# Optimization experiments

Measured on AMD Instinct MI355X. Metric: run time of the kernel, lower is better.

## Reference

```python
import jax, jax.numpy as jnp
import numpy as np

N_SAMPLES = 131072
N_FEATURES = 64
N_TREES = 64
DEPTH = 12                      # complete binary trees
N_INTERNAL = 2 ** DEPTH - 1     # 4095 internal nodes per tree
N_LEAVES = 2 ** DEPTH           # 4096 leaves per tree
N_CLASSES = 8


def setup_inputs() -> dict:
    key = jax.random.key(0)
    k1, k2, k3, k4 = jax.random.split(key, 4)
    X = jax.random.normal(k1, (N_SAMPLES, N_FEATURES), dtype=jnp.float32)
    # flattened complete-binary-tree parameters (FIL-style layout)
    features = jax.random.randint(k2, (N_TREES, N_INTERNAL), 0, N_FEATURES, dtype=jnp.int32)
    thresholds = jax.random.normal(k3, (N_TREES, N_INTERNAL), dtype=jnp.float32)
    leaf_values = jax.random.randint(k4, (N_TREES, N_LEAVES), 0, N_CLASSES, dtype=jnp.int32)
    return {"X": X, "features": features, "thresholds": thresholds, "leaf_values": leaf_values}


def reference(X, features, thresholds, leaf_values):
    # X: [N, F]; features/thresholds: [T, 2^D-1]; leaf_values: [T, 2^D]
    N = X.shape[0]
    row = jnp.arange(N)[None, :]                      # [1, N] broadcasts over trees
    node = jnp.zeros((N_TREES, N), dtype=jnp.int32)   # all samples start at root of every tree
    for _ in range(DEPTH):                            # fixed-depth traversal, fully vectorized
        f = jnp.take_along_axis(features, node, axis=1)      # [T, N] feature id per (tree, sample)
        t = jnp.take_along_axis(thresholds, node, axis=1)    # [T, N]
        xv = X[row, f]                                        # [T, N] gathered feature values
        node = 2 * node + 1 + (xv > t).astype(jnp.int32)      # go left (<=) or right (>)
    leaf_idx = node - N_INTERNAL                              # [T, N] in [0, 2^D)
    preds = jnp.take_along_axis(leaf_values, leaf_idx, axis=1)  # [T, N] per-tree class votes
    # majority vote == torch.mode over trees; argmax returns smallest class on ties,
    # matching torch.mode's smallest-modal-value convention
    counts = (preds[:, :, None] == jnp.arange(N_CLASSES)[None, None, :]).sum(axis=0)  # [N, C]
    return jnp.argmax(counts, axis=1)  # [N] final class predictions
```

## Files before the change

kernel.cpp:

```cpp
#include <hip/hip_runtime.h>


constexpr int kSamples  = 131072;
constexpr int kFeat     = 64;
constexpr int kTrees    = 64;
constexpr int kInternal = 4095;
constexpr int kClasses  = 8;

constexpr int TPB  = 1024;
constexpr int SPB  = 256;
constexpr int XSTR = 256;
constexpr int XLDS_BYTES = kFeat * XSTR * 4;
constexpr int ILP  = 8;
constexpr int TREES_PER_THREAD = 16;

struct Pair  { float thr0, thrL, thrR; unsigned meta; };
struct Sub16 { float thr10, thrL, thrR; unsigned meta; };

__global__ __launch_bounds__(256) void pack_pairs_kernel(
    const int* __restrict__ features, const float* __restrict__ thresholds,
    Pair* __restrict__ pairsA)
{
    int i = blockIdx.x * 256 + threadIdx.x;
    if (i >= kTrees * 341) return;
    int t = i / 341;
    int e = i - t * 341;
    int p, m;
    if      (e < 1)  { p = 0; m = e; }
    else if (e < 5)  { p = 1; m = e - 1; }
    else if (e < 21) { p = 2; m = e - 5; }
    else if (e < 85) { p = 3; m = e - 21; }
    else             { p = 4; m = e - 85; }
    int g0 = (1 << (2 * p)) - 1 + m;
    int b  = t * kInternal;
    Pair pr;
    pr.thr0 = thresholds[b + g0];
    pr.thrL = thresholds[b + 2 * g0 + 1];
    pr.thrR = thresholds[b + 2 * g0 + 2];
    pr.meta = (unsigned)features[b + g0]
            | ((unsigned)features[b + 2 * g0 + 1] << 6)
            | ((unsigned)features[b + 2 * g0 + 2] << 12);
    pairsA[(t << 9) + e] = pr;
}

__global__ __launch_bounds__(256) void pack_sub_kernel(
    const int* __restrict__ features, const float* __restrict__ thresholds,
    const int* __restrict__ leaf_values, Sub16* __restrict__ subsA)
{
    int i = blockIdx.x * 256 + threadIdx.x;
    if (i >= kTrees * 1024) return;
    int t = i >> 10;
    int j = i & 1023;
    int n10 = 1023 + j;
    int b   = t * kInternal;
    Sub16 sb;
    sb.thr10 = thresholds[b + n10];
    sb.thrL  = thresholds[b + 2 * n10 + 1];
    sb.thrR  = thresholds[b + 2 * n10 + 2];
    const int* lv = leaf_values + ((t << 12) + 4 * j);
    sb.meta = (unsigned)features[b + n10]
            | ((unsigned)features[b + 2 * n10 + 1] << 6)
            | ((unsigned)features[b + 2 * n10 + 2] << 12)
            | ((unsigned)lv[0] << 18) | ((unsigned)lv[1] << 21)
            | ((unsigned)lv[2] << 24) | ((unsigned)lv[3] << 27);
    subsA[(t << 10) + j] = sb;
}

__global__ __launch_bounds__(TPB, 8) void forest_kernel(
    const float* __restrict__ X,
    const Pair*  __restrict__ pairsA,
    const Sub16* __restrict__ subsA,
    int* __restrict__ out)
{
    extern __shared__ float xs[];
    const int tid  = threadIdx.x;
    const int s    = tid & (SPB - 1);
    const int h    = tid >> 8;
    const int base = blockIdx.x * SPB;

    {
        const float4* Xr = (const float4*)(X + (size_t)(base + s) * kFeat) + h * 4;
        #pragma unroll
        for (int k = 0; k < 4; ++k) {
            float4 v = Xr[k];
            int f0 = (h * 4 + k) * 4;
            xs[(f0 + 0) * XSTR + s] = v.x;
            xs[(f0 + 1) * XSTR + s] = v.y;
            xs[(f0 + 2) * XSTR + s] = v.z;
            xs[(f0 + 3) * XSTR + s] = v.w;
        }
    }
    __syncthreads();

    const char* xb = (const char*)xs + (s << 2);
    unsigned long long votes = 0ull;

    const int mofs[4] = {0, 1, 5, 21};

    const int tbeg = h * TREES_PER_THREAD;
    for (int t0 = tbeg; t0 < tbeg + TREES_PER_THREAD; t0 += ILP) {
        int m[ILP];
        #pragma unroll
        for (int j = 0; j < ILP; ++j) m[j] = 0;

        #pragma unroll
        for (int p = 0; p < 4; ++p) {
            #pragma unroll
            for (int j = 0; j < ILP; ++j) {
                Pair pr = pairsA[((t0 + j) << 9) + mofs[p] + m[j]];
                float x0 = *(const float*)(xb + ((pr.meta & 63u) << 10));
                int c0 = x0 > pr.thr0 ? 1 : 0;
                float thr1     = c0 ? pr.thrR : pr.thrL;
                unsigned fsel  = c0 ? (pr.meta >> 12) : (pr.meta >> 6);
                float x1 = *(const float*)(xb + ((fsel & 63u) << 10));
                int c1 = x1 > thr1 ? 1 : 0;
                m[j] = 4 * m[j] + 2 * c0 + c1;
            }
        }

        #pragma unroll
        for (int j = 0; j < ILP; ++j) {
            Pair pr = pairsA[((t0 + j) << 9) + 85 + m[j]];
            float x0 = *(const float*)(xb + ((pr.meta & 63u) << 10));
            int c0 = x0 > pr.thr0 ? 1 : 0;
            float thr1     = c0 ? pr.thrR : pr.thrL;
            unsigned fsel  = c0 ? (pr.meta >> 12) : (pr.meta >> 6);
            float x1 = *(const float*)(xb + ((fsel & 63u) << 10));
            int c1 = x1 > thr1 ? 1 : 0;
            m[j] = 4 * m[j] + 2 * c0 + c1;
        }

        #pragma unroll
        for (int j = 0; j < ILP; ++j) {
            Sub16 sb = subsA[((t0 + j) << 10) + m[j]];
            unsigned mt = sb.meta;
            float x0 = *(const float*)(xb + ((mt & 63u) << 10));
            int c0 = x0 > sb.thr10 ? 1 : 0;
            float thr1    = c0 ? sb.thrR : sb.thrL;
            unsigned fsel = c0 ? (mt >> 12) : (mt >> 6);
            float x1 = *(const float*)(xb + ((fsel & 63u) << 10));
            int c1 = x1 > thr1 ? 1 : 0;
            int cls = (mt >> (18 + 3 * ((c0 << 1) | c1))) & 7;
            votes += 1ull << (cls << 3);
        }
    }

    __syncthreads();
    unsigned long long* vbuf = (unsigned long long*)xs;
    if (h != 0) vbuf[(h - 1) * SPB + s] = votes;
    __syncthreads();
    if (h == 0) {
        votes += vbuf[s] + vbuf[SPB + s] + vbuf[2 * SPB + s];
        int best = 0;
        int bc   = (int)(votes & 0xFFull);
        #pragma unroll
        for (int c = 1; c < kClasses; ++c) {
            int cnt = (int)((votes >> (c * 8)) & 0xFFull);
            if (cnt > bc) { bc = cnt; best = c; }
        }
        out[base + s] = best;
    }
}

extern "C" void kernel_launch(void* const* d_in, const int* in_sizes, int n_in,
                              void* d_out, int out_size, void* d_ws, size_t ws_size,
                              hipStream_t stream) {
    const float* X          = (const float*)d_in[0];
    const int*   features   = (const int*)d_in[1];
    const float* thresholds = (const float*)d_in[2];
    const int*   leaves     = (const int*)d_in[3];
    int*         out        = (int*)d_out;

    Pair*  pairsA = (Pair*)d_ws;
    Sub16* subsA  = (Sub16*)((char*)d_ws + (kTrees << 13));

    (void)hipFuncSetAttribute((const void*)forest_kernel,
                              hipFuncAttributeMaxDynamicSharedMemorySize,
                              XLDS_BYTES);

    pack_pairs_kernel<<<(kTrees * 341 + 255) / 256, 256, 0, stream>>>(
        features, thresholds, pairsA);
    pack_sub_kernel<<<(kTrees * 1024 + 255) / 256, 256, 0, stream>>>(
        features, thresholds, leaves, subsA);
    forest_kernel<<<kSamples / SPB, TPB, XLDS_BYTES, stream>>>(
        X, pairsA, subsA, out);
}
```

Baseline: 116.6 us.

## Fuse packing and traversal into one persistent cooperative kernel with grid sync

Merges the two tree-packing kernels and the forest traversal kernel into a single cooperative launch. Blocks first pack pairs and subtrees with a grid-stride loop, load their first X chunk into LDS, then wait at a grid-wide barrier before traversing. Blocks are persistent and loop over sample chunks. This removes two extra kernel launches and their inter-kernel gaps, at the cost of a grid sync, a grid sized from occupancy (which assumes 256 CUs), and reduced overlap between blocks.

```diff
diff --git a/kernel.cpp b/kernel.cpp
--- a/kernel.cpp
+++ b/kernel.cpp
@@ -1,4 +1,7 @@
 #include <hip/hip_runtime.h>
+#include <hip/hip_cooperative_groups.h>
+
+namespace cg = cooperative_groups;
 
 
 constexpr int kSamples  = 131072;
@@ -13,73 +16,72 @@
 constexpr int XLDS_BYTES = kFeat * XSTR * 4;
 constexpr int ILP  = 8;
 constexpr int TREES_PER_THREAD = 16;
+constexpr int NCHUNKS = kSamples / SPB;
 
 struct Pair  { float thr0, thrL, thrR; unsigned meta; };
 struct Sub16 { float thr10, thrL, thrR; unsigned meta; };
 
-__global__ __launch_bounds__(256) void pack_pairs_kernel(
-    const int* __restrict__ features, const float* __restrict__ thresholds,
-    Pair* __restrict__ pairsA)
-{
-    int i = blockIdx.x * 256 + threadIdx.x;
-    if (i >= kTrees * 341) return;
-    int t = i / 341;
-    int e = i - t * 341;
-    int p, m;
-    if      (e < 1)  { p = 0; m = e; }
-    else if (e < 5)  { p = 1; m = e - 1; }
-    else if (e < 21) { p = 2; m = e - 5; }
-    else if (e < 85) { p = 3; m = e - 21; }
-    else             { p = 4; m = e - 85; }
-    int g0 = (1 << (2 * p)) - 1 + m;
-    int b  = t * kInternal;
-    Pair pr;
-    pr.thr0 = thresholds[b + g0];
-    pr.thrL = thresholds[b + 2 * g0 + 1];
-    pr.thrR = thresholds[b + 2 * g0 + 2];
-    pr.meta = (unsigned)features[b + g0]
-            | ((unsigned)features[b + 2 * g0 + 1] << 6)
-            | ((unsigned)features[b + 2 * g0 + 2] << 12);
-    pairsA[(t << 9) + e] = pr;
-}
-
-__global__ __launch_bounds__(256) void pack_sub_kernel(
-    const int* __restrict__ features, const float* __restrict__ thresholds,
-    const int* __restrict__ leaf_values, Sub16* __restrict__ subsA)
-{
-    int i = blockIdx.x * 256 + threadIdx.x;
-    if (i >= kTrees * 1024) return;
-    int t = i >> 10;
-    int j = i & 1023;
-    int n10 = 1023 + j;
-    int b   = t * kInternal;
-    Sub16 sb;
-    sb.thr10 = thresholds[b + n10];
-    sb.thrL  = thresholds[b + 2 * n10 + 1];
-    sb.thrR  = thresholds[b + 2 * n10 + 2];
-    const int* lv = leaf_values + ((t << 12) + 4 * j);
-    sb.meta = (unsigned)features[b + n10]
-            | ((unsigned)features[b + 2 * n10 + 1] << 6)
-            | ((unsigned)features[b + 2 * n10 + 2] << 12)
-            | ((unsigned)lv[0] << 18) | ((unsigned)lv[1] << 21)
-            | ((unsigned)lv[2] << 24) | ((unsigned)lv[3] << 27);
-    subsA[(t << 10) + j] = sb;
-}
-
-__global__ __launch_bounds__(TPB, 8) void forest_kernel(
+constexpr int kPairItems = kTrees * 341;
+constexpr int kSubItems  = kTrees * 1024;
+constexpr int kPackItems = kPairItems + kSubItems;
+
+__global__ __launch_bounds__(TPB, 8) void forest_all(
     const float* __restrict__ X,
-    const Pair*  __restrict__ pairsA,
-    const Sub16* __restrict__ subsA,
-    int* __restrict__ out)
+    const int*   __restrict__ features,
+    const float* __restrict__ thresholds,
+    const int*   __restrict__ leaf_values,
+    Pair*        __restrict__ pairsA,
+    Sub16*       __restrict__ subsA,
+    int*         __restrict__ out)
 {
     extern __shared__ float xs[];
-    const int tid  = threadIdx.x;
-    const int s    = tid & (SPB - 1);
-    const int h    = tid >> 8;
-    const int base = blockIdx.x * SPB;
+    const int tid = threadIdx.x;
+    const int s   = tid & (SPB - 1);
+    const int h   = tid >> 8;
+
+    for (int g = blockIdx.x * TPB + tid; g < kPackItems; g += gridDim.x * TPB) {
+        if (g < kPairItems) {
+            int t = g / 341;
+            int e = g - t * 341;
+            int p, m;
+            if      (e < 1)  { p = 0; m = e; }
+            else if (e < 5)  { p = 1; m = e - 1; }
+            else if (e < 21) { p = 2; m = e - 5; }
+            else if (e < 85) { p = 3; m = e - 21; }
+            else             { p = 4; m = e - 85; }
+            int g0 = (1 << (2 * p)) - 1 + m;
+            int b  = t * kInternal;
+            Pair pr;
+            pr.thr0 = thresholds[b + g0];
+            pr.thrL = thresholds[b + 2 * g0 + 1];
+            pr.thrR = thresholds[b + 2 * g0 + 2];
+            pr.meta = (unsigned)features[b + g0]
+                    | ((unsigned)features[b + 2 * g0 + 1] << 6)
+                    | ((unsigned)features[b + 2 * g0 + 2] << 12);
+            pairsA[(t << 9) + e] = pr;
+        } else {
+            int i2 = g - kPairItems;
+            int t = i2 >> 10;
+            int j = i2 & 1023;
+            int n10 = 1023 + j;
+            int b   = t * kInternal;
+            Sub16 sb;
+            sb.thr10 = thresholds[b + n10];
+            sb.thrL  = thresholds[b + 2 * n10 + 1];
+            sb.thrR  = thresholds[b + 2 * n10 + 2];
+            const int* lv = leaf_values + ((t << 12) + 4 * j);
+            sb.meta = (unsigned)features[b + n10]
+                    | ((unsigned)features[b + 2 * n10 + 1] << 6)
+                    | ((unsigned)features[b + 2 * n10 + 2] << 12)
+                    | ((unsigned)lv[0] << 18) | ((unsigned)lv[1] << 21)
+                    | ((unsigned)lv[2] << 24) | ((unsigned)lv[3] << 27);
+            subsA[(t << 10) + j] = sb;
+        }
+    }
 
     {
-        const float4* Xr = (const float4*)(X + (size_t)(base + s) * kFeat) + h * 4;
+        const int base0 = blockIdx.x * SPB;
+        const float4* Xr = (const float4*)(X + (size_t)(base0 + s) * kFeat) + h * 4;
         #pragma unroll
         for (int k = 0; k < 4; ++k) {
             float4 v = Xr[k];
@@ -90,24 +92,56 @@
             xs[(f0 + 3) * XSTR + s] = v.w;
         }
     }
-    __syncthreads();
+
+    __threadfence();
+    cg::this_grid().sync();
 
     const char* xb = (const char*)xs + (s << 2);
-    unsigned long long votes = 0ull;
-
     const int mofs[4] = {0, 1, 5, 21};
 
-    const int tbeg = h * TREES_PER_THREAD;
-    for (int t0 = tbeg; t0 < tbeg + TREES_PER_THREAD; t0 += ILP) {
-        int m[ILP];
-        #pragma unroll
-        for (int j = 0; j < ILP; ++j) m[j] = 0;
-
-        #pragma unroll
-        for (int p = 0; p < 4; ++p) {
+    bool first = true;
+    for (int chunk = blockIdx.x; chunk < NCHUNKS; chunk += (int)gridDim.x) {
+        const int base = chunk * SPB;
+
+        if (!first) {
+            const float4* Xr = (const float4*)(X + (size_t)(base + s) * kFeat) + h * 4;
+            #pragma unroll
+            for (int k = 0; k < 4; ++k) {
+                float4 v = Xr[k];
+                int f0 = (h * 4 + k) * 4;
+                xs[(f0 + 0) * XSTR + s] = v.x;
+                xs[(f0 + 1) * XSTR + s] = v.y;
+                xs[(f0 + 2) * XSTR + s] = v.z;
+                xs[(f0 + 3) * XSTR + s] = v.w;
+            }
+        }
+        __syncthreads();
+
+        unsigned long long votes = 0ull;
+        const int tbeg = h * TREES_PER_THREAD;
+        for (int t0 = tbeg; t0 < tbeg + TREES_PER_THREAD; t0 += ILP) {
+            int m[ILP];
+            #pragma unroll
+            for (int j = 0; j < ILP; ++j) m[j] = 0;
+
+            #pragma unroll
+            for (int p = 0; p < 4; ++p) {
+                #pragma unroll
+                for (int j = 0; j < ILP; ++j) {
+                    Pair pr = pairsA[((t0 + j) << 9) + mofs[p] + m[j]];
+                    float x0 = *(const float*)(xb + ((pr.meta & 63u) << 10));
+                    int c0 = x0 > pr.thr0 ? 1 : 0;
+                    float thr1     = c0 ? pr.thrR : pr.thrL;
+                    unsigned fsel  = c0 ? (pr.meta >> 12) : (pr.meta >> 6);
+                    float x1 = *(const float*)(xb + ((fsel & 63u) << 10));
+                    int c1 = x1 > thr1 ? 1 : 0;
+                    m[j] = 4 * m[j] + 2 * c0 + c1;
+                }
+            }
+
             #pragma unroll
             for (int j = 0; j < ILP; ++j) {
-                Pair pr = pairsA[((t0 + j) << 9) + mofs[p] + m[j]];
+                Pair pr = pairsA[((t0 + j) << 9) + 85 + m[j]];
                 float x0 = *(const float*)(xb + ((pr.meta & 63u) << 10));
                 int c0 = x0 > pr.thr0 ? 1 : 0;
                 float thr1     = c0 ? pr.thrR : pr.thrL;
@@ -116,49 +150,39 @@
                 int c1 = x1 > thr1 ? 1 : 0;
                 m[j] = 4 * m[j] + 2 * c0 + c1;
             }
-        }
-
-        #pragma unroll
-        for (int j = 0; j < ILP; ++j) {
-            Pair pr = pairsA[((t0 + j) << 9) + 85 + m[j]];
-            float x0 = *(const float*)(xb + ((pr.meta & 63u) << 10));
-            int c0 = x0 > pr.thr0 ? 1 : 0;
-            float thr1     = c0 ? pr.thrR : pr.thrL;
-            unsigned fsel  = c0 ? (pr.meta >> 12) : (pr.meta >> 6);
-            float x1 = *(const float*)(xb + ((fsel & 63u) << 10));
-            int c1 = x1 > thr1 ? 1 : 0;
-            m[j] = 4 * m[j] + 2 * c0 + c1;
-        }
-
-        #pragma unroll
-        for (int j = 0; j < ILP; ++j) {
-            Sub16 sb = subsA[((t0 + j) << 10) + m[j]];
-            unsigned mt = sb.meta;
-            float x0 = *(const float*)(xb + ((mt & 63u) << 10));
-            int c0 = x0 > sb.thr10 ? 1 : 0;
-            float thr1    = c0 ? sb.thrR : sb.thrL;
-            unsigned fsel = c0 ? (mt >> 12) : (mt >> 6);
-            float x1 = *(const float*)(xb + ((fsel & 63u) << 10));
-            int c1 = x1 > thr1 ? 1 : 0;
-            int cls = (mt >> (18 + 3 * ((c0 << 1) | c1))) & 7;
-            votes += 1ull << (cls << 3);
-        }
-    }
-
-    __syncthreads();
-    unsigned long long* vbuf = (unsigned long long*)xs;
-    if (h != 0) vbuf[(h - 1) * SPB + s] = votes;
-    __syncthreads();
-    if (h == 0) {
-        votes += vbuf[s] + vbuf[SPB + s] + vbuf[2 * SPB + s];
-        int best = 0;
-        int bc   = (int)(votes & 0xFFull);
-        #pragma unroll
-        for (int c = 1; c < kClasses; ++c) {
-            int cnt = (int)((votes >> (c * 8)) & 0xFFull);
-            if (cnt > bc) { bc = cnt; best = c; }
-        }
-        out[base + s] = best;
+
+            #pragma unroll
+            for (int j = 0; j < ILP; ++j) {
+                Sub16 sb = subsA[((t0 + j) << 10) + m[j]];
+                unsigned mt = sb.meta;
+                float x0 = *(const float*)(xb + ((mt & 63u) << 10));
+                int c0 = x0 > sb.thr10 ? 1 : 0;
+                float thr1    = c0 ? sb.thrR : sb.thrL;
+                unsigned fsel = c0 ? (mt >> 12) : (mt >> 6);
+                float x1 = *(const float*)(xb + ((fsel & 63u) << 10));
+                int c1 = x1 > thr1 ? 1 : 0;
+                int cls = (mt >> (18 + 3 * ((c0 << 1) | c1))) & 7;
+                votes += 1ull << (cls << 3);
+            }
+        }
+
+        __syncthreads();
+        unsigned long long* vbuf = (unsigned long long*)xs;
+        if (h != 0) vbuf[(h - 1) * SPB + s] = votes;
+        __syncthreads();
+        if (h == 0) {
+            votes += vbuf[s] + vbuf[SPB + s] + vbuf[2 * SPB + s];
+            int best = 0;
+            int bc   = (int)(votes & 0xFFull);
+            #pragma unroll
+            for (int c = 1; c < kClasses; ++c) {
+                int cnt = (int)((votes >> (c * 8)) & 0xFFull);
+                if (cnt > bc) { bc = cnt; best = c; }
+            }
+            out[base + s] = best;
+        }
+        __syncthreads();
+        first = false;
     }
 }
 
@@ -174,14 +198,19 @@
     Pair*  pairsA = (Pair*)d_ws;
     Sub16* subsA  = (Sub16*)((char*)d_ws + (kTrees << 13));
 
-    (void)hipFuncSetAttribute((const void*)forest_kernel,
+    (void)hipFuncSetAttribute((const void*)forest_all,
                               hipFuncAttributeMaxDynamicSharedMemorySize,
                               XLDS_BYTES);
 
-    pack_pairs_kernel<<<(kTrees * 341 + 255) / 256, 256, 0, stream>>>(
-        features, thresholds, pairsA);
-    pack_sub_kernel<<<(kTrees * 1024 + 255) / 256, 256, 0, stream>>>(
-        features, thresholds, leaves, subsA);
-    forest_kernel<<<kSamples / SPB, TPB, XLDS_BYTES, stream>>>(
-        X, pairsA, subsA, out);
+    int maxB = 0;
+    (void)hipOccupancyMaxActiveBlocksPerMultiprocessor(
+        &maxB, (const void*)forest_all, TPB, XLDS_BYTES);
+    if (maxB < 1) maxB = 1;
+    unsigned grid = (unsigned)maxB * 256u;
+    if (grid > (unsigned)NCHUNKS) grid = (unsigned)NCHUNKS;
+
+    void* args[] = {(void*)&X, (void*)&features, (void*)&thresholds, (void*)&leaves,
+                    (void*)&pairsA, (void*)&subsA, (void*)&out};
+    (void)hipLaunchCooperativeKernel((const void*)forest_all, dim3(grid), dim3(TPB),
+                                     args, (unsigned)XLDS_BYTES, stream);
 }
```

Measured after the change: 283.4 us. +143.1%, slower.

## Fuse tree packing and forest traversal into one cooperative kernel with grid sync

Applied to the files above, without the earlier changes.

Merges the two packing kernels and the traversal kernel into a single cooperative kernel. Each block first does its share of the pair/sub-table packing and loads its X tile into LDS, then a grid-wide sync makes the packed tables visible to every block before traversal starts. This removes two extra kernel launches and the gaps between them, and overlaps the X tile load with packing. In exchange it adds a grid barrier and relies on all 512 blocks being resident at once; if the cooperative launch fails, the original three-kernel path is used.

```diff
diff --git a/kernel.cpp b/kernel.cpp
--- a/kernel.cpp
+++ b/kernel.cpp
@@ -1,4 +1,7 @@
 #include <hip/hip_runtime.h>
+#include <hip/hip_cooperative_groups.h>
+
+namespace cg = cooperative_groups;
 
 
 constexpr int kSamples  = 131072;
@@ -13,9 +16,158 @@
 constexpr int XLDS_BYTES = kFeat * XSTR * 4;
 constexpr int ILP  = 8;
 constexpr int TREES_PER_THREAD = 16;
+constexpr int NCHUNKS = kSamples / SPB;
 
 struct Pair  { float thr0, thrL, thrR; unsigned meta; };
 struct Sub16 { float thr10, thrL, thrR; unsigned meta; };
+
+constexpr int kPairItems = kTrees * 341;
+constexpr int kSubItems  = kTrees * 1024;
+constexpr int kPackItems = kPairItems + kSubItems;
+
+
+__global__ __launch_bounds__(TPB, 8) void forest_all(
+    const float* __restrict__ X,
+    const int*   __restrict__ features,
+    const float* __restrict__ thresholds,
+    const int*   __restrict__ leaf_values,
+    Pair*        __restrict__ pairsA,
+    Sub16*       __restrict__ subsA,
+    int*         __restrict__ out)
+{
+    extern __shared__ float xs[];
+    const int tid  = threadIdx.x;
+    const int s    = tid & (SPB - 1);
+    const int h    = tid >> 8;
+    const int base = blockIdx.x * SPB;
+
+    {
+        const int g = blockIdx.x * TPB + tid;
+        if (g < kPairItems) {
+            int t = g / 341;
+            int e = g - t * 341;
+            int p, m;
+            if      (e < 1)  { p = 0; m = e; }
+            else if (e < 5)  { p = 1; m = e - 1; }
+            else if (e < 21) { p = 2; m = e - 5; }
+            else if (e < 85) { p = 3; m = e - 21; }
+            else             { p = 4; m = e - 85; }
+            int g0 = (1 << (2 * p)) - 1 + m;
+            int b  = t * kInternal;
+            Pair pr;
+            pr.thr0 = thresholds[b + g0];
+            pr.thrL = thresholds[b + 2 * g0 + 1];
+            pr.thrR = thresholds[b + 2 * g0 + 2];
+            pr.meta = (unsigned)features[b + g0]
+                    | ((unsigned)features[b + 2 * g0 + 1] << 6)
+                    | ((unsigned)features[b + 2 * g0 + 2] << 12);
+            pairsA[(t << 9) + e] = pr;
+        } else if (g < kPackItems) {
+            int i2 = g - kPairItems;
+            int t = i2 >> 10;
+            int j = i2 & 1023;
+            int n10 = 1023 + j;
+            int b   = t * kInternal;
+            Sub16 sb;
+            sb.thr10 = thresholds[b + n10];
+            sb.thrL  = thresholds[b + 2 * n10 + 1];
+            sb.thrR  = thresholds[b + 2 * n10 + 2];
+            const int* lv = leaf_values + ((t << 12) + 4 * j);
+            sb.meta = (unsigned)features[b + n10]
+                    | ((unsigned)features[b + 2 * n10 + 1] << 6)
+                    | ((unsigned)features[b + 2 * n10 + 2] << 12)
+                    | ((unsigned)lv[0] << 18) | ((unsigned)lv[1] << 21)
+                    | ((unsigned)lv[2] << 24) | ((unsigned)lv[3] << 27);
+            subsA[(t << 10) + j] = sb;
+        }
+    }
+
+    {
+        const float4* Xr = (const float4*)(X + (size_t)(base + s) * kFeat) + h * 4;
+        #pragma unroll
+        for (int k = 0; k < 4; ++k) {
+            float4 v = Xr[k];
+            int f0 = (h * 4 + k) * 4;
+            xs[(f0 + 0) * XSTR + s] = v.x;
+            xs[(f0 + 1) * XSTR + s] = v.y;
+            xs[(f0 + 2) * XSTR + s] = v.z;
+            xs[(f0 + 3) * XSTR + s] = v.w;
+        }
+    }
+
+    __threadfence();
+    cg::this_grid().sync();
+
+    const char* xb = (const char*)xs + (s << 2);
+    unsigned long long votes = 0ull;
+
+    const int mofs[4] = {0, 1, 5, 21};
+
+    const int tbeg = h * TREES_PER_THREAD;
+    for (int t0 = tbeg; t0 < tbeg + TREES_PER_THREAD; t0 += ILP) {
+        int m[ILP];
+        #pragma unroll
+        for (int j = 0; j < ILP; ++j) m[j] = 0;
+
+        #pragma unroll
+        for (int p = 0; p < 4; ++p) {
+            #pragma unroll
+            for (int j = 0; j < ILP; ++j) {
+                Pair pr = pairsA[((t0 + j) << 9) + mofs[p] + m[j]];
+                float x0 = *(const float*)(xb + ((pr.meta & 63u) << 10));
+                int c0 = x0 > pr.thr0 ? 1 : 0;
+                float thr1     = c0 ? pr.thrR : pr.thrL;
+                unsigned fsel  = c0 ? (pr.meta >> 12) : (pr.meta >> 6);
+                float x1 = *(const float*)(xb + ((fsel & 63u) << 10));
+                int c1 = x1 > thr1 ? 1 : 0;
+                m[j] = 4 * m[j] + 2 * c0 + c1;
+            }
+        }
+
+        #pragma unroll
+        for (int j = 0; j < ILP; ++j) {
+            Pair pr = pairsA[((t0 + j) << 9) + 85 + m[j]];
+            float x0 = *(const float*)(xb + ((pr.meta & 63u) << 10));
+            int c0 = x0 > pr.thr0 ? 1 : 0;
+            float thr1     = c0 ? pr.thrR : pr.thrL;
+            unsigned fsel  = c0 ? (pr.meta >> 12) : (pr.meta >> 6);
+            float x1 = *(const float*)(xb + ((fsel & 63u) << 10));
+            int c1 = x1 > thr1 ? 1 : 0;
+            m[j] = 4 * m[j] + 2 * c0 + c1;
+        }
+
+        #pragma unroll
+        for (int j = 0; j < ILP; ++j) {
+            Sub16 sb = subsA[((t0 + j) << 10) + m[j]];
+            unsigned mt = sb.meta;
+            float x0 = *(const float*)(xb + ((mt & 63u) << 10));
+            int c0 = x0 > sb.thr10 ? 1 : 0;
+            float thr1    = c0 ? sb.thrR : sb.thrL;
+            unsigned fsel = c0 ? (mt >> 12) : (mt >> 6);
+            float x1 = *(const float*)(xb + ((fsel & 63u) << 10));
+            int c1 = x1 > thr1 ? 1 : 0;
+            int cls = (mt >> (18 + 3 * ((c0 << 1) | c1))) & 7;
+            votes += 1ull << (cls << 3);
+        }
+    }
+
+    __syncthreads();
+    unsigned long long* vbuf = (unsigned long long*)xs;
+    if (h != 0) vbuf[(h - 1) * SPB + s] = votes;
+    __syncthreads();
+    if (h == 0) {
+        votes += vbuf[s] + vbuf[SPB + s] + vbuf[2 * SPB + s];
+        int best = 0;
+        int bc   = (int)(votes & 0xFFull);
+        #pragma unroll
+        for (int c = 1; c < kClasses; ++c) {
+            int cnt = (int)((votes >> (c * 8)) & 0xFFull);
+            if (cnt > bc) { bc = cnt; best = c; }
+        }
+        out[base + s] = best;
+    }
+}
+
 
 __global__ __launch_bounds__(256) void pack_pairs_kernel(
     const int* __restrict__ features, const float* __restrict__ thresholds,
@@ -94,7 +246,6 @@
 
     const char* xb = (const char*)xs + (s << 2);
     unsigned long long votes = 0ull;
-
     const int mofs[4] = {0, 1, 5, 21};
 
     const int tbeg = h * TREES_PER_THREAD;
@@ -174,9 +325,25 @@
     Pair*  pairsA = (Pair*)d_ws;
     Sub16* subsA  = (Sub16*)((char*)d_ws + (kTrees << 13));
 
+    (void)hipFuncSetAttribute((const void*)forest_all,
+                              hipFuncAttributeMaxDynamicSharedMemorySize,
+                              XLDS_BYTES);
     (void)hipFuncSetAttribute((const void*)forest_kernel,
                               hipFuncAttributeMaxDynamicSharedMemorySize,
                               XLDS_BYTES);
+
+    int maxB = 0;
+    (void)hipOccupancyMaxActiveBlocksPerMultiprocessor(
+        &maxB, (const void*)forest_all, TPB, XLDS_BYTES);
+
+    if (maxB >= 2) {
+        void* args[] = {(void*)&X, (void*)&features, (void*)&thresholds,
+                        (void*)&leaves, (void*)&pairsA, (void*)&subsA, (void*)&out};
+        hipError_t e = hipLaunchCooperativeKernel((const void*)forest_all,
+                                                  dim3(NCHUNKS), dim3(TPB),
+                                                  args, (unsigned)XLDS_BYTES, stream);
+        if (e == hipSuccess) return;
+    }
 
     pack_pairs_kernel<<<(kTrees * 341 + 255) / 256, 256, 0, stream>>>(
         features, thresholds, pairsA);
```

Measured after the change: 117.7 us. About the same (+1.0%).

## Walk all trees per thread in lockstep with per-tree prefetch and merged pack

Applied to the files above, without the earlier changes.

Replaces the four-way tree split per sample with one thread per sample that walks all 64 trees sequentially. The cross-thread vote reduction goes away, and the whole block touches the same tree at the same time so it stays hot in cache. Each iteration prefetches the next tree's packed nodes cooperatively and ends with a block barrier to keep threads in lockstep. The two pack kernels are merged into one launch. In exchange it drops the 8-tree ILP and adds 64 barriers, 128KB of LDS per block, and fewer concurrent waves to hide load latency.

```diff
diff --git a/kernel.cpp b/kernel.cpp
--- a/kernel.cpp
+++ b/kernel.cpp
@@ -7,159 +7,146 @@
 constexpr int kInternal = 4095;
 constexpr int kClasses  = 8;
 
-constexpr int TPB  = 1024;
-constexpr int SPB  = 256;
-constexpr int XSTR = 256;
-constexpr int XLDS_BYTES = kFeat * XSTR * 4;
-constexpr int ILP  = 8;
-constexpr int TREES_PER_THREAD = 16;
+constexpr int TPB = 512;
+constexpr int SPB = 512;
+constexpr int XLDS_BYTES = kFeat * SPB * 4;
 
 struct Pair  { float thr0, thrL, thrR; unsigned meta; };
 struct Sub16 { float thr10, thrL, thrR; unsigned meta; };
 
-__global__ __launch_bounds__(256) void pack_pairs_kernel(
+constexpr int kPairItems = kTrees * 341;
+constexpr int kSubItems  = kTrees * 1024;
+constexpr int kPackItems = kPairItems + kSubItems;
+
+
+__global__ __launch_bounds__(256) void pack_kernel(
     const int* __restrict__ features, const float* __restrict__ thresholds,
-    Pair* __restrict__ pairsA)
+    const int* __restrict__ leaf_values,
+    Pair* __restrict__ pairsA, Sub16* __restrict__ subsA)
 {
-    int i = blockIdx.x * 256 + threadIdx.x;
-    if (i >= kTrees * 341) return;
-    int t = i / 341;
-    int e = i - t * 341;
-    int p, m;
-    if      (e < 1)  { p = 0; m = e; }
-    else if (e < 5)  { p = 1; m = e - 1; }
-    else if (e < 21) { p = 2; m = e - 5; }
-    else if (e < 85) { p = 3; m = e - 21; }
-    else             { p = 4; m = e - 85; }
-    int g0 = (1 << (2 * p)) - 1 + m;
-    int b  = t * kInternal;
-    Pair pr;
-    pr.thr0 = thresholds[b + g0];
-    pr.thrL = thresholds[b + 2 * g0 + 1];
-    pr.thrR = thresholds[b + 2 * g0 + 2];
-    pr.meta = (unsigned)features[b + g0]
-            | ((unsigned)features[b + 2 * g0 + 1] << 6)
-            | ((unsigned)features[b + 2 * g0 + 2] << 12);
-    pairsA[(t << 9) + e] = pr;
+    int g = blockIdx.x * 256 + threadIdx.x;
+    if (g < kPairItems) {
+        int t = g / 341;
+        int e = g - t * 341;
+        int p, m;
+        if      (e < 1)  { p = 0; m = e; }
+        else if (e < 5)  { p = 1; m = e - 1; }
+        else if (e < 21) { p = 2; m = e - 5; }
+        else if (e < 85) { p = 3; m = e - 21; }
+        else             { p = 4; m = e - 85; }
+        int g0 = (1 << (2 * p)) - 1 + m;
+        int b  = t * kInternal;
+        Pair pr;
+        pr.thr0 = thresholds[b + g0];
+        pr.thrL = thresholds[b + 2 * g0 + 1];
+        pr.thrR = thresholds[b + 2 * g0 + 2];
+        pr.meta = (unsigned)features[b + g0]
+                | ((unsigned)features[b + 2 * g0 + 1] << 6)
+                | ((unsigned)features[b + 2 * g0 + 2] << 12);
+        pairsA[(t << 9) + e] = pr;
+    } else if (g < kPackItems) {
+        int i2 = g - kPairItems;
+        int t = i2 >> 10;
+        int j = i2 & 1023;
+        int n10 = 1023 + j;
+        int b   = t * kInternal;
+        Sub16 sb;
+        sb.thr10 = thresholds[b + n10];
+        sb.thrL  = thresholds[b + 2 * n10 + 1];
+        sb.thrR  = thresholds[b + 2 * n10 + 2];
+        const int* lv = leaf_values + ((t << 12) + 4 * j);
+        sb.meta = (unsigned)features[b + n10]
+                | ((unsigned)features[b + 2 * n10 + 1] << 6)
+                | ((unsigned)features[b + 2 * n10 + 2] << 12)
+                | ((unsigned)lv[0] << 18) | ((unsigned)lv[1] << 21)
+                | ((unsigned)lv[2] << 24) | ((unsigned)lv[3] << 27);
+        subsA[(t << 10) + j] = sb;
+    }
 }
 
-__global__ __launch_bounds__(256) void pack_sub_kernel(
-    const int* __restrict__ features, const float* __restrict__ thresholds,
-    const int* __restrict__ leaf_values, Sub16* __restrict__ subsA)
+
+__device__ __forceinline__ void prefetch_tree(
+    const Pair* pairsA, const Sub16* subsA, int t, int s)
 {
-    int i = blockIdx.x * 256 + threadIdx.x;
-    if (i >= kTrees * 1024) return;
-    int t = i >> 10;
-    int j = i & 1023;
-    int n10 = 1023 + j;
-    int b   = t * kInternal;
-    Sub16 sb;
-    sb.thr10 = thresholds[b + n10];
-    sb.thrL  = thresholds[b + 2 * n10 + 1];
-    sb.thrR  = thresholds[b + 2 * n10 + 2];
-    const int* lv = leaf_values + ((t << 12) + 4 * j);
-    sb.meta = (unsigned)features[b + n10]
-            | ((unsigned)features[b + 2 * n10 + 1] << 6)
-            | ((unsigned)features[b + 2 * n10 + 2] << 12)
-            | ((unsigned)lv[0] << 18) | ((unsigned)lv[1] << 21)
-            | ((unsigned)lv[2] << 24) | ((unsigned)lv[3] << 27);
-    subsA[(t << 10) + j] = sb;
+    if (s < 342) {
+        const char* pf = (s < 86)
+            ? ((const char*)pairsA + (t << 13) + (s << 6))
+            : ((const char*)subsA  + (t << 14) + ((s - 86) << 6));
+        unsigned pv = *(const unsigned*)pf;
+        asm volatile("" :: "v"(pv));
+    }
 }
 
-__global__ __launch_bounds__(TPB, 8) void forest_kernel(
+__global__ __launch_bounds__(TPB, 2) void forest_kernel(
     const float* __restrict__ X,
     const Pair*  __restrict__ pairsA,
     const Sub16* __restrict__ subsA,
     int* __restrict__ out)
 {
     extern __shared__ float xs[];
-    const int tid  = threadIdx.x;
-    const int s    = tid & (SPB - 1);
-    const int h    = tid >> 8;
+    const int s    = threadIdx.x;
     const int base = blockIdx.x * SPB;
 
     {
-        const float4* Xr = (const float4*)(X + (size_t)(base + s) * kFeat) + h * 4;
+        const float4* Xr = (const float4*)(X + (size_t)(base + s) * kFeat);
         #pragma unroll
-        for (int k = 0; k < 4; ++k) {
+        for (int k = 0; k < 16; ++k) {
             float4 v = Xr[k];
-            int f0 = (h * 4 + k) * 4;
-            xs[(f0 + 0) * XSTR + s] = v.x;
-            xs[(f0 + 1) * XSTR + s] = v.y;
-            xs[(f0 + 2) * XSTR + s] = v.z;
-            xs[(f0 + 3) * XSTR + s] = v.w;
+            int f0 = k * 4;
+            xs[(f0 + 0) * SPB + s] = v.x;
+            xs[(f0 + 1) * SPB + s] = v.y;
+            xs[(f0 + 2) * SPB + s] = v.z;
+            xs[(f0 + 3) * SPB + s] = v.w;
         }
     }
+    prefetch_tree(pairsA, subsA, 0, s);
     __syncthreads();
 
     const char* xb = (const char*)xs + (s << 2);
     unsigned long long votes = 0ull;
 
-    const int mofs[4] = {0, 1, 5, 21};
+    const int mofs[5] = {0, 1, 5, 21, 85};
 
-    const int tbeg = h * TREES_PER_THREAD;
-    for (int t0 = tbeg; t0 < tbeg + TREES_PER_THREAD; t0 += ILP) {
-        int m[ILP];
+    for (int t = 0; t < kTrees; ++t) {
+        if (t + 1 < kTrees) prefetch_tree(pairsA, subsA, t + 1, s);
+
+        int m = 0;
         #pragma unroll
-        for (int j = 0; j < ILP; ++j) m[j] = 0;
-
-        #pragma unroll
-        for (int p = 0; p < 4; ++p) {
-            #pragma unroll
-            for (int j = 0; j < ILP; ++j) {
-                Pair pr = pairsA[((t0 + j) << 9) + mofs[p] + m[j]];
-                float x0 = *(const float*)(xb + ((pr.meta & 63u) << 10));
-                int c0 = x0 > pr.thr0 ? 1 : 0;
-                float thr1     = c0 ? pr.thrR : pr.thrL;
-                unsigned fsel  = c0 ? (pr.meta >> 12) : (pr.meta >> 6);
-                float x1 = *(const float*)(xb + ((fsel & 63u) << 10));
-                int c1 = x1 > thr1 ? 1 : 0;
-                m[j] = 4 * m[j] + 2 * c0 + c1;
-            }
-        }
-
-        #pragma unroll
-        for (int j = 0; j < ILP; ++j) {
-            Pair pr = pairsA[((t0 + j) << 9) + 85 + m[j]];
-            float x0 = *(const float*)(xb + ((pr.meta & 63u) << 10));
+        for (int p = 0; p < 5; ++p) {
+            Pair pr = pairsA[(t << 9) + mofs[p] + m];
+            float x0 = *(const float*)(xb + ((pr.meta & 63u) << 11));
             int c0 = x0 > pr.thr0 ? 1 : 0;
             float thr1     = c0 ? pr.thrR : pr.thrL;
             unsigned fsel  = c0 ? (pr.meta >> 12) : (pr.meta >> 6);
-            float x1 = *(const float*)(xb + ((fsel & 63u) << 10));
+            float x1 = *(const float*)(xb + ((fsel & 63u) << 11));
             int c1 = x1 > thr1 ? 1 : 0;
-            m[j] = 4 * m[j] + 2 * c0 + c1;
+            m = 4 * m + 2 * c0 + c1;
         }
 
-        #pragma unroll
-        for (int j = 0; j < ILP; ++j) {
-            Sub16 sb = subsA[((t0 + j) << 10) + m[j]];
+        {
+            Sub16 sb = subsA[(t << 10) + m];
             unsigned mt = sb.meta;
-            float x0 = *(const float*)(xb + ((mt & 63u) << 10));
+            float x0 = *(const float*)(xb + ((mt & 63u) << 11));
             int c0 = x0 > sb.thr10 ? 1 : 0;
             float thr1    = c0 ? sb.thrR : sb.thrL;
             unsigned fsel = c0 ? (mt >> 12) : (mt >> 6);
-            float x1 = *(const float*)(xb + ((fsel & 63u) << 10));
+            float x1 = *(const float*)(xb + ((fsel & 63u) << 11));
             int c1 = x1 > thr1 ? 1 : 0;
             int cls = (mt >> (18 + 3 * ((c0 << 1) | c1))) & 7;
             votes += 1ull << (cls << 3);
         }
+
+        __syncthreads();
     }
 
-    __syncthreads();
-    unsigned long long* vbuf = (unsigned long long*)xs;
-    if (h != 0) vbuf[(h - 1) * SPB + s] = votes;
-    __syncthreads();
-    if (h == 0) {
-        votes += vbuf[s] + vbuf[SPB + s] + vbuf[2 * SPB + s];
-        int best = 0;
-        int bc   = (int)(votes & 0xFFull);
-        #pragma unroll
-        for (int c = 1; c < kClasses; ++c) {
-            int cnt = (int)((votes >> (c * 8)) & 0xFFull);
-            if (cnt > bc) { bc = cnt; best = c; }
-        }
-        out[base + s] = best;
+    int best = 0;
+    int bc   = (int)(votes & 0xFFull);
+    #pragma unroll
+    for (int c = 1; c < kClasses; ++c) {
+        int cnt = (int)((votes >> (c * 8)) & 0xFFull);
+        if (cnt > bc) { bc = cnt; best = c; }
     }
+    out[base + s] = best;
 }
 
 extern "C" void kernel_launch(void* const* d_in, const int* in_sizes, int n_in,
@@ -178,10 +165,8 @@
                               hipFuncAttributeMaxDynamicSharedMemorySize,
                               XLDS_BYTES);
 
-    pack_pairs_kernel<<<(kTrees * 341 + 255) / 256, 256, 0, stream>>>(
-        features, thresholds, pairsA);
-    pack_sub_kernel<<<(kTrees * 1024 + 255) / 256, 256, 0, stream>>>(
-        features, thresholds, leaves, subsA);
+    pack_kernel<<<(kPackItems + 255) / 256, 256, 0, stream>>>(
+        features, thresholds, leaves, pairsA, subsA);
     forest_kernel<<<kSamples / SPB, TPB, XLDS_BYTES, stream>>>(
         X, pairsA, subsA, out);
 }
```

New measurement: 175.9 us. 1.51x slower.
